# Kernel tuning notes

Hardware: AMD Instinct MI355X
Metric: run time of the kernel (lower is better)

## Reference

```python
import jax, jax.numpy as jnp
import numpy as np

IGNORE_INDEX = 255
NUM_CLASSES = 6


def setup_inputs() -> dict:
    key = jax.random.key(0)
    k1, k2 = jax.random.split(key)
    B, C, H, W = 16, 256, 128, 128
    x = jax.random.normal(k1, (B, C, H, W), dtype=jnp.float32)
    gt = jax.random.randint(k2, (B, 1, H, W), 0, NUM_CLASSES, dtype=jnp.int32)
    return {"x": x, "gt": gt}


def reference(x, gt):
    # x: (B, C, H, W) float32; gt: (B, 1, H, W) int
    B, C, H, W = x.shape
    K = NUM_CLASSES
    # F.interpolate(gt.float(), size=(H,W), mode='nearest') is identity here
    label = gt[:, 0]                                  # (B, H, W)
    not_ignore = (label != IGNORE_INDEX)              # (B, H, W) bool
    label = jnp.where(not_ignore, label, 0)           # zero out ignored pixels
    # one-hot with ignored positions masked to all-zero rows
    oh = jax.nn.one_hot(label, K, dtype=jnp.float32)  # (B, H, W, K)
    oh = oh * not_ignore[..., None].astype(jnp.float32)
    oh_flat = oh.reshape(B, H * W, K)                 # (B, N, K)
    x_flat = x.reshape(B, C, H * W)                   # (B, C, N)
    # per-class pixel counts (count_nonzero of one-hot == its sum)
    counts = jnp.sum(oh_flat, axis=1)                 # (B, K)
    counts = jnp.maximum(counts, 1.0)
    # masked sum pooling per class: (B, K, N) @ (B, N, C) -> (B, K, C)
    center = jnp.einsum('bnk,bcn->bkc', oh_flat, x_flat)
    center = center / counts[:, :, None]
    return center
```

## Files before the change

kernel.cpp:

```cpp
#include <hip/hip_runtime.h>
#include <hip/hip_bf16.h>

#define BATCH 16
#define CHAN  256
#define HW    16384
#define NCLS  6

__global__ __launch_bounds__(256)
void gt2center_kernel(const float* __restrict__ x,
                      const int*   __restrict__ gt,
                      float*       __restrict__ out) {
    const int bc = blockIdx.x;
    const int b  = bc >> 8;
    const int c  = bc & 255;
    const float* __restrict__ xp = x  + (size_t)bc * HW;
    const int*   __restrict__ gp = gt + (size_t)b  * HW;
    const int t = threadIdx.x;

    float s[NCLS];
    int   cnt[NCLS];
#pragma unroll
    for (int k = 0; k < NCLS; ++k) { s[k] = 0.0f; cnt[k] = 0; }

#pragma unroll
    for (int i = 0; i < 16; ++i) {
        const int n = i * 1024 + t * 4;
        const float4 v = *reinterpret_cast<const float4*>(xp + n);
        const int4   L = *reinterpret_cast<const int4*>(gp + n);
#pragma unroll
        for (int k = 0; k < NCLS; ++k) {
            s[k] += (L.x == k) ? v.x : 0.0f;
            s[k] += (L.y == k) ? v.y : 0.0f;
            s[k] += (L.z == k) ? v.z : 0.0f;
            s[k] += (L.w == k) ? v.w : 0.0f;
            cnt[k] += (L.x == k) + (L.y == k) + (L.z == k) + (L.w == k);
        }
    }

#pragma unroll
    for (int off = 32; off >= 1; off >>= 1) {
#pragma unroll
        for (int k = 0; k < NCLS; ++k) {
            s[k]   += __shfl_xor(s[k],   off, 64);
            cnt[k] += __shfl_xor(cnt[k], off, 64);
        }
    }

    __shared__ float ls[4][NCLS];
    __shared__ int   lc[4][NCLS];
    const int wave = t >> 6, lane = t & 63;
    if (lane == 0) {
#pragma unroll
        for (int k = 0; k < NCLS; ++k) { ls[wave][k] = s[k]; lc[wave][k] = cnt[k]; }
    }
    __syncthreads();

    if (t < NCLS) {
        const float ssum = ls[0][t] + ls[1][t] + ls[2][t] + ls[3][t];
        const int   csum = lc[0][t] + lc[1][t] + lc[2][t] + lc[3][t];
        const float d = (csum > 1) ? (float)csum : 1.0f;
        out[((size_t)b * NCLS + t) * CHAN + c] = ssum / d;
    }
}

extern "C" void kernel_launch(void* const* d_in, const int* in_sizes, int n_in,
                              void* d_out, int out_size, void* d_ws, size_t ws_size,
                              hipStream_t stream) {
    const float* x  = (const float*)d_in[0];
    const int*   gt = (const int*)d_in[1];
    float*       out = (float*)d_out;
    gt2center_kernel<<<BATCH * CHAN, 256, 0, stream>>>(x, gt, out);
}
```

Baseline: 49.69 us.

## Precompute per-class counts in separate kernel and use nontemporal x loads

Adds a small kernel that computes inverse per-class pixel counts once per batch and stores them in workspace. The main kernel then drops its redundant per-channel counting and shuffle reductions and multiplies by the precomputed reciprocal. It also loads x with nontemporal hints so the streamed data does not pollute cache and gt stays resident. The cost is an extra kernel launch and a serial dependency between the two kernels.

```diff
diff --git a/kernel.cpp b/kernel.cpp
--- a/kernel.cpp
+++ b/kernel.cpp
@@ -6,9 +6,49 @@
 #define HW    16384
 #define NCLS  6
 
+typedef float  f32x4 __attribute__((ext_vector_type(4)));
+typedef int    i32x4 __attribute__((ext_vector_type(4)));
+
+__global__ __launch_bounds__(256)
+void count_kernel(const int* __restrict__ gt, float* __restrict__ invcnt) {
+    const int b = blockIdx.x;
+    const int t = threadIdx.x;
+    const int* __restrict__ gp = gt + (size_t)b * HW;
+
+    int cnt[NCLS];
+#pragma unroll
+    for (int k = 0; k < NCLS; ++k) cnt[k] = 0;
+
+#pragma unroll
+    for (int i = 0; i < 16; ++i) {
+        const i32x4 L = *reinterpret_cast<const i32x4*>(gp + i * 1024 + t * 4);
+#pragma unroll
+        for (int k = 0; k < NCLS; ++k)
+            cnt[k] += (L.x == k) + (L.y == k) + (L.z == k) + (L.w == k);
+    }
+
+#pragma unroll
+    for (int off = 32; off >= 1; off >>= 1)
+#pragma unroll
+        for (int k = 0; k < NCLS; ++k) cnt[k] += __shfl_xor(cnt[k], off, 64);
+
+    __shared__ int lc[4][NCLS];
+    const int wave = t >> 6, lane = t & 63;
+    if (lane == 0)
+#pragma unroll
+        for (int k = 0; k < NCLS; ++k) lc[wave][k] = cnt[k];
+    __syncthreads();
+
+    if (t < NCLS) {
+        const int csum = lc[0][t] + lc[1][t] + lc[2][t] + lc[3][t];
+        invcnt[b * NCLS + t] = 1.0f / (float)((csum > 1) ? csum : 1);
+    }
+}
+
 __global__ __launch_bounds__(256)
 void gt2center_kernel(const float* __restrict__ x,
                       const int*   __restrict__ gt,
+                      const float* __restrict__ invcnt,
                       float*       __restrict__ out) {
     const int bc = blockIdx.x;
     const int b  = bc >> 8;
@@ -18,56 +58,51 @@
     const int t = threadIdx.x;
 
     float s[NCLS];
-    int   cnt[NCLS];
 #pragma unroll
-    for (int k = 0; k < NCLS; ++k) { s[k] = 0.0f; cnt[k] = 0; }
+    for (int k = 0; k < NCLS; ++k) s[k] = 0.0f;
 
 #pragma unroll
     for (int i = 0; i < 16; ++i) {
         const int n = i * 1024 + t * 4;
-        const float4 v = *reinterpret_cast<const float4*>(xp + n);
-        const int4   L = *reinterpret_cast<const int4*>(gp + n);
+        const f32x4 v = __builtin_nontemporal_load(
+            reinterpret_cast<const f32x4*>(xp + n));
+        const i32x4 L = *reinterpret_cast<const i32x4*>(gp + n);
 #pragma unroll
         for (int k = 0; k < NCLS; ++k) {
             s[k] += (L.x == k) ? v.x : 0.0f;
             s[k] += (L.y == k) ? v.y : 0.0f;
             s[k] += (L.z == k) ? v.z : 0.0f;
             s[k] += (L.w == k) ? v.w : 0.0f;
-            cnt[k] += (L.x == k) + (L.y == k) + (L.z == k) + (L.w == k);
         }
     }
 
 #pragma unroll
-    for (int off = 32; off >= 1; off >>= 1) {
+    for (int off = 32; off >= 1; off >>= 1)
 #pragma unroll
-        for (int k = 0; k < NCLS; ++k) {
-            s[k]   += __shfl_xor(s[k],   off, 64);
-            cnt[k] += __shfl_xor(cnt[k], off, 64);
-        }
-    }
+        for (int k = 0; k < NCLS; ++k)
+            s[k] += __shfl_xor(s[k], off, 64);
 
     __shared__ float ls[4][NCLS];
-    __shared__ int   lc[4][NCLS];
     const int wave = t >> 6, lane = t & 63;
-    if (lane == 0) {
+    if (lane == 0)
 #pragma unroll
-        for (int k = 0; k < NCLS; ++k) { ls[wave][k] = s[k]; lc[wave][k] = cnt[k]; }
-    }
+        for (int k = 0; k < NCLS; ++k) ls[wave][k] = s[k];
     __syncthreads();
 
     if (t < NCLS) {
         const float ssum = ls[0][t] + ls[1][t] + ls[2][t] + ls[3][t];
-        const int   csum = lc[0][t] + lc[1][t] + lc[2][t] + lc[3][t];
-        const float d = (csum > 1) ? (float)csum : 1.0f;
-        out[((size_t)b * NCLS + t) * CHAN + c] = ssum / d;
+        out[((size_t)b * NCLS + t) * CHAN + c] = ssum * invcnt[b * NCLS + t];
     }
 }
 
 extern "C" void kernel_launch(void* const* d_in, const int* in_sizes, int n_in,
                               void* d_out, int out_size, void* d_ws, size_t ws_size,
                               hipStream_t stream) {
-    const float* x  = (const float*)d_in[0];
-    const int*   gt = (const int*)d_in[1];
+    const float* x   = (const float*)d_in[0];
+    const int*   gt  = (const int*)d_in[1];
     float*       out = (float*)d_out;
-    gt2center_kernel<<<BATCH * CHAN, 256, 0, stream>>>(x, gt, out);
+    float*       invcnt = (float*)d_ws;
+
+    count_kernel<<<BATCH, 256, 0, stream>>>(gt, invcnt);
+    gt2center_kernel<<<BATCH * CHAN, 256, 0, stream>>>(x, gt, invcnt, out);
 }
```

Result: slower. 55.64 us (+12.0%).
